# Performance work log

Measured on AMD Instinct MI355X. Metric: run time of the kernel, lower is better.

The kernel has to match this reference:

```python
import jax, jax.numpy as jnp
import numpy as np

B, C, H, W = 256, 1024, 7, 7
D_HID, N_CLS = 768, 5

def setup_inputs() -> dict:
    key = jax.random.key(0)
    k1, k2, k3, k4, k5 = jax.random.split(key, 5)
    flat = C * H * W  # 50176
    return {
        "features": jax.random.normal(k1, (B, C, H, W), dtype=jnp.float32),
        "W1": jax.random.normal(k2, (D_HID, flat), dtype=jnp.float32) * 0.02,
        "b1": jax.random.normal(k3, (D_HID,), dtype=jnp.float32) * 0.02,
        "W2": jax.random.normal(k4, (N_CLS, D_HID), dtype=jnp.float32) * 0.02,
        "b2": jax.random.normal(k5, (N_CLS,), dtype=jnp.float32) * 0.02,
    }

def reference(features, W1, b1, W2, b2):
    # PCAM: per-(batch, channel) global max over spatial dims, broadcast-multiplied
    # back onto the feature map. Replaces the torch Python double loop with one
    # fused reduce-max + elementwise multiply.
    ch_max = jnp.max(features, axis=(2, 3), keepdims=True)  # [B, C, 1, 1]
    pcams = features * ch_max                               # [B, C, H, W]
    flat = pcams.reshape(pcams.shape[0], -1)                # [B, C*H*W]
    h = jax.nn.relu(flat @ W1.T + b1)                       # [B, 768]
    logits = h @ W2.T + b2                                  # [B, num_classes]
    return (logits, features)
```

## Files before the change

kernel.cpp:

```cpp
#include <hip/hip_runtime.h>
#include <hip/hip_bf16.h>

#define B_SZ   256
#define C_SZ   1024
#define HW     49
#define KDIM   50176
#define DHID   768
#define NCLS   5

typedef __bf16 bf16x8 __attribute__((ext_vector_type(8)));
typedef __bf16 bf16x4 __attribute__((ext_vector_type(4)));
typedef float  f32x4  __attribute__((ext_vector_type(4)));

#define GLOAD_LDS16(gsrc, ldst) \
  __builtin_amdgcn_global_load_lds((__attribute__((address_space(1))) void*)(gsrc), \
                                   (__attribute__((address_space(3))) void*)(ldst), 16, 0, 0)

__global__ __launch_bounds__(256) void pcam_kernel(const float* __restrict__ feat,
                                                   float* __restrict__ feat_out,
                                                   __bf16* __restrict__ pcam) {
  __shared__ float sv[1568];
  __shared__ float smax[32];
  const int tid = threadIdx.x;
  const size_t base = (size_t)blockIdx.x * 1568;

  const float4* src4 = (const float4*)(feat + base);
  float4* dst4 = (float4*)(feat_out + base);
  #pragma unroll
  for (int i = 0; i < 2; ++i) {
    int idx = tid + i * 256;
    if (idx < 392) {
      float4 v = src4[idx];
      dst4[idx] = v;
      ((float4*)sv)[idx] = v;
    }
  }
  __syncthreads();

  {
    const int r = tid >> 3, p = tid & 7;
    float mx = -INFINITY;
    for (int i = p; i < HW; i += 8) mx = fmaxf(mx, sv[r * HW + i]);
    #pragma unroll
    for (int off = 1; off < 8; off <<= 1) mx = fmaxf(mx, __shfl_xor(mx, off));
    if (p == 0) smax[r] = mx;
  }
  __syncthreads();

  for (int i = tid; i < 1568; i += 256) {
    int r = (i * 1338) >> 16;
    float v = sv[i] * smax[r];
    pcam[base + i] = (__bf16)v;
  }
}

#define BM 256
#define BN 128
#define BK 64
#define NT 6
#define KSPLIT 42
#define KSTEPS 784

__global__ __launch_bounds__(512, 2) void gemm1_kernel(const __bf16* __restrict__ pcam,
                                                       const float* __restrict__ W1,
                                                       float* __restrict__ h_acc) {
  __shared__ __bf16 Asm[BM * BK];
  __shared__ __bf16 Bsm[BN * BK];

  const int tid  = threadIdx.x;
  const int lane = tid & 63;
  const int w    = tid >> 6;
  const int wm   = w >> 1;
  const int wn   = w & 1;
  const int n0   = blockIdx.x * BN;
  const int ks   = blockIdx.y;
  const int s0   = (ks * KSTEPS) / KSPLIT;
  const int s1   = ((ks + 1) * KSTEPS) / KSPLIT;

  f32x4 acc[4][4];
  #pragma unroll
  for (int i = 0; i < 4; ++i)
    #pragma unroll
    for (int j = 0; j < 4; ++j) acc[i][j] = f32x4{0.f, 0.f, 0.f, 0.f};

  for (int s = s0; s < s1; ++s) {
    const int k0 = s * BK;

    #pragma unroll
    for (int it = 0; it < 4; ++it) {
      const int q   = it * 512 + tid;
      const int m   = q >> 3;
      const int kbp = q & 7;
      const int kbl = kbp ^ (m & 7);
      const __bf16* src = pcam + (size_t)m * KDIM + k0 + kbl * 8;
      __bf16* ldsb = Asm + (size_t)(it * 512 + w * 64) * 8;
      GLOAD_LDS16(src, ldsb);
    }

    #pragma unroll
    for (int it = 0; it < 4; ++it) {
      const int f  = it * 512 + tid;
      const int n  = f >> 4;
      const int kq = f & 15;
      const float4 v = *(const float4*)(W1 + (size_t)(n0 + n) * KDIM + k0 + kq * 4);
      bf16x4 bv;
      bv[0] = (__bf16)v.x; bv[1] = (__bf16)v.y; bv[2] = (__bf16)v.z; bv[3] = (__bf16)v.w;
      const int kb   = kq >> 1;
      const int phys = n * 128 + (((kb ^ (n & 7)) << 4) | ((kq & 1) << 3));
      *(bf16x4*)((char*)Bsm + phys) = bv;
    }
    __syncthreads();

    #pragma unroll
    for (int ksub = 0; ksub < 2; ++ksub) {
      bf16x8 af[4], bfr[4];
      const int kb = ksub * 4 + (lane >> 4);
      #pragma unroll
      for (int i = 0; i < 4; ++i) {
        const int m = wm * 64 + i * 16 + (lane & 15);
        af[i] = *(const bf16x8*)((const char*)Asm + m * 128 + ((kb ^ (m & 7)) << 4));
      }
      #pragma unroll
      for (int j = 0; j < 4; ++j) {
        const int n = wn * 64 + j * 16 + (lane & 15);
        bfr[j] = *(const bf16x8*)((const char*)Bsm + n * 128 + ((kb ^ (n & 7)) << 4));
      }
      #pragma unroll
      for (int i = 0; i < 4; ++i)
        #pragma unroll
        for (int j = 0; j < 4; ++j)
          acc[i][j] = __builtin_amdgcn_mfma_f32_16x16x32_bf16(af[i], bfr[j], acc[i][j], 0, 0, 0);
    }
    __syncthreads();
  }

  #pragma unroll
  for (int i = 0; i < 4; ++i) {
    const int mb = wm * 64 + i * 16 + (lane >> 4) * 4;
    #pragma unroll
    for (int j = 0; j < 4; ++j) {
      const int n = n0 + wn * 64 + j * 16 + (lane & 15);
      #pragma unroll
      for (int r = 0; r < 4; ++r)
        unsafeAtomicAdd(&h_acc[(size_t)(mb + r) * DHID + n], acc[i][j][r]);
    }
  }
}

__global__ __launch_bounds__(64) void head_kernel(const float* __restrict__ h_acc,
                                                  const float* __restrict__ b1,
                                                  const float* __restrict__ W2,
                                                  const float* __restrict__ b2,
                                                  float* __restrict__ logits) {
  const int m = blockIdx.x;
  const int lane = threadIdx.x;
  float hv[12];
  #pragma unroll
  for (int j = 0; j < 12; ++j) {
    float v = h_acc[(size_t)m * DHID + j * 64 + lane] + b1[j * 64 + lane];
    hv[j] = v > 0.f ? v : 0.f;
  }
  #pragma unroll
  for (int c = 0; c < NCLS; ++c) {
    float s = 0.f;
    #pragma unroll
    for (int j = 0; j < 12; ++j) s += hv[j] * W2[c * DHID + j * 64 + lane];
    #pragma unroll
    for (int off = 32; off > 0; off >>= 1) s += __shfl_xor(s, off);
    if (lane == 0) logits[m * NCLS + c] = s + b2[c];
  }
}

extern "C" void kernel_launch(void* const* d_in, const int* in_sizes, int n_in,
                              void* d_out, int out_size, void* d_ws, size_t ws_size,
                              hipStream_t stream) {
  const float* feat = (const float*)d_in[0];
  const float* W1   = (const float*)d_in[1];
  const float* b1   = (const float*)d_in[2];
  const float* W2   = (const float*)d_in[3];
  const float* b2   = (const float*)d_in[4];

  float* logits   = (float*)d_out;
  float* feat_out = (float*)d_out + (size_t)B_SZ * NCLS;

  __bf16* pcam  = (__bf16*)d_ws;
  float*  h_acc = (float*)((char*)d_ws + (size_t)B_SZ * KDIM * 2);

  hipMemsetAsync(h_acc, 0, (size_t)B_SZ * DHID * sizeof(float), stream);
  pcam_kernel<<<(B_SZ * C_SZ) / 32, 256, 0, stream>>>(feat, feat_out, pcam);
  gemm1_kernel<<<dim3(NT, KSPLIT), 512, 0, stream>>>(pcam, W1, h_acc);
  head_kernel<<<B_SZ, 64, 0, stream>>>(h_acc, b1, W2, b2, logits);
}
```

Baseline: 109.3 us.

## Double-buffer GEMM LDS stages and split M into two tiles

The GEMM now uses a 128x128 block tile instead of 256x128, which doubles the grid to 12x42 blocks. It also double-buffers A and B in LDS, prefetching the next k-step (an async global->LDS load for A, a register load for W1) while the current step computes. The goal is to hide global-memory latency and raise occupancy (launch bounds 512,4) for this memory-bound fp32-W1 stream. The cost is that each W1 tile is now read by two blocks, and the extra blocks issue more atomic adds.

Result: slower. 112.4 us (+2.8%).

```diff
diff --git a/kernel.cpp b/kernel.cpp
--- a/kernel.cpp
+++ b/kernel.cpp
@@ -54,97 +54,133 @@
   }
 }
 
-#define BM 256
+#define BM 128
 #define BN 128
 #define BK 64
+#define MT 2
 #define NT 6
 #define KSPLIT 42
 #define KSTEPS 784
 
-__global__ __launch_bounds__(512, 2) void gemm1_kernel(const __bf16* __restrict__ pcam,
+__global__ __launch_bounds__(512, 4) void gemm1_kernel(const __bf16* __restrict__ pcam,
                                                        const float* __restrict__ W1,
                                                        float* __restrict__ h_acc) {
-  __shared__ __bf16 Asm[BM * BK];
-  __shared__ __bf16 Bsm[BN * BK];
+  __shared__ __bf16 Asm[2][BM * BK];
+  __shared__ __bf16 Bsm[2][BN * BK];
 
   const int tid  = threadIdx.x;
   const int lane = tid & 63;
   const int w    = tid >> 6;
-  const int wm   = w >> 1;
-  const int wn   = w & 1;
-  const int n0   = blockIdx.x * BN;
+  const int wm   = w >> 2;
+  const int wn   = w & 3;
+  const int bx   = blockIdx.x;
+  const int m0   = (bx & 1) * BM;
+  const int n0   = (bx >> 1) * BN;
   const int ks   = blockIdx.y;
   const int s0   = (ks * KSTEPS) / KSPLIT;
   const int s1   = ((ks + 1) * KSTEPS) / KSPLIT;
 
-  f32x4 acc[4][4];
+  const int nb = tid >> 4;
+  const int kq = tid & 15;
+  const int kb = kq >> 1;
+  const int sub = (kq & 1) << 3;
+
+  f32x4 acc[4][2];
   #pragma unroll
   for (int i = 0; i < 4; ++i)
     #pragma unroll
-    for (int j = 0; j < 4; ++j) acc[i][j] = f32x4{0.f, 0.f, 0.f, 0.f};
-
+    for (int j = 0; j < 2; ++j) acc[i][j] = f32x4{0.f, 0.f, 0.f, 0.f};
+
+  float4 br0, br1, br2, br3;
+
+#define LOAD_B(s) do { \
+    const size_t koff_ = (size_t)(s) * BK + kq * 4; \
+    br0 = *(const float4*)(W1 + (size_t)(n0 + 0  + nb) * KDIM + koff_); \
+    br1 = *(const float4*)(W1 + (size_t)(n0 + 32 + nb) * KDIM + koff_); \
+    br2 = *(const float4*)(W1 + (size_t)(n0 + 64 + nb) * KDIM + koff_); \
+    br3 = *(const float4*)(W1 + (size_t)(n0 + 96 + nb) * KDIM + koff_); \
+  } while (0)
+
+#define STAGE_A(bi, s) do { \
+    const int k0_ = (s) * BK; \
+    _Pragma("unroll") \
+    for (int it = 0; it < 2; ++it) { \
+      const int q   = it * 512 + tid; \
+      const int m   = q >> 3; \
+      const int kbl = (q & 7) ^ (m & 7); \
+      const __bf16* src = pcam + (size_t)(m0 + m) * KDIM + k0_ + kbl * 8; \
+      GLOAD_LDS16(src, &Asm[bi][(size_t)(it * 512 + w * 64) * 8]); \
+    } \
+  } while (0)
+
+#define WRITE_B(bi) do { \
+    _Pragma("unroll") \
+    for (int it = 0; it < 4; ++it) { \
+      const float4 v = (it == 0) ? br0 : (it == 1) ? br1 : (it == 2) ? br2 : br3; \
+      bf16x4 bv; \
+      bv[0] = (__bf16)v.x; bv[1] = (__bf16)v.y; bv[2] = (__bf16)v.z; bv[3] = (__bf16)v.w; \
+      const int n = it * 32 + nb; \
+      const int phys = n * 128 + (((kb ^ (n & 7)) << 4) | sub); \
+      *(bf16x4*)((char*)Bsm[bi] + phys) = bv; \
+    } \
+  } while (0)
+
+#define COMPUTE(bi) do { \
+    _Pragma("unroll") \
+    for (int ksub = 0; ksub < 2; ++ksub) { \
+      bf16x8 af[4], bfr[2]; \
+      const int kb2 = ksub * 4 + (lane >> 4); \
+      _Pragma("unroll") \
+      for (int i = 0; i < 4; ++i) { \
+        const int m = wm * 64 + i * 16 + (lane & 15); \
+        af[i] = *(const bf16x8*)((const char*)Asm[bi] + m * 128 + ((kb2 ^ (m & 7)) << 4)); \
+      } \
+      _Pragma("unroll") \
+      for (int j = 0; j < 2; ++j) { \
+        const int n = wn * 32 + j * 16 + (lane & 15); \
+        bfr[j] = *(const bf16x8*)((const char*)Bsm[bi] + n * 128 + ((kb2 ^ (n & 7)) << 4)); \
+      } \
+      _Pragma("unroll") \
+      for (int i = 0; i < 4; ++i) \
+        _Pragma("unroll") \
+        for (int j = 0; j < 2; ++j) \
+          acc[i][j] = __builtin_amdgcn_mfma_f32_16x16x32_bf16(af[i], bfr[j], acc[i][j], 0, 0, 0); \
+    } \
+  } while (0)
+
+  LOAD_B(s0);
+  STAGE_A(0, s0);
+  WRITE_B(0);
+  __syncthreads();
+
+  int buf = 0;
   for (int s = s0; s < s1; ++s) {
-    const int k0 = s * BK;
-
-    #pragma unroll
-    for (int it = 0; it < 4; ++it) {
-      const int q   = it * 512 + tid;
-      const int m   = q >> 3;
-      const int kbp = q & 7;
-      const int kbl = kbp ^ (m & 7);
-      const __bf16* src = pcam + (size_t)m * KDIM + k0 + kbl * 8;
-      __bf16* ldsb = Asm + (size_t)(it * 512 + w * 64) * 8;
-      GLOAD_LDS16(src, ldsb);
+    const int nxt = s + 1;
+    if (nxt < s1) {
+      LOAD_B(nxt);
+      STAGE_A(buf ^ 1, nxt);
     }
-
-    #pragma unroll
-    for (int it = 0; it < 4; ++it) {
-      const int f  = it * 512 + tid;
-      const int n  = f >> 4;
-      const int kq = f & 15;
-      const float4 v = *(const float4*)(W1 + (size_t)(n0 + n) * KDIM + k0 + kq * 4);
-      bf16x4 bv;
-      bv[0] = (__bf16)v.x; bv[1] = (__bf16)v.y; bv[2] = (__bf16)v.z; bv[3] = (__bf16)v.w;
-      const int kb   = kq >> 1;
-      const int phys = n * 128 + (((kb ^ (n & 7)) << 4) | ((kq & 1) << 3));
-      *(bf16x4*)((char*)Bsm + phys) = bv;
-    }
+    COMPUTE(buf);
+    if (nxt < s1) WRITE_B(buf ^ 1);
     __syncthreads();
-
-    #pragma unroll
-    for (int ksub = 0; ksub < 2; ++ksub) {
-      bf16x8 af[4], bfr[4];
-      const int kb = ksub * 4 + (lane >> 4);
-      #pragma unroll
-      for (int i = 0; i < 4; ++i) {
-        const int m = wm * 64 + i * 16 + (lane & 15);
-        af[i] = *(const bf16x8*)((const char*)Asm + m * 128 + ((kb ^ (m & 7)) << 4));
-      }
-      #pragma unroll
-      for (int j = 0; j < 4; ++j) {
-        const int n = wn * 64 + j * 16 + (lane & 15);
-        bfr[j] = *(const bf16x8*)((const char*)Bsm + n * 128 + ((kb ^ (n & 7)) << 4));
-      }
-      #pragma unroll
-      for (int i = 0; i < 4; ++i)
-        #pragma unroll
-        for (int j = 0; j < 4; ++j)
-          acc[i][j] = __builtin_amdgcn_mfma_f32_16x16x32_bf16(af[i], bfr[j], acc[i][j], 0, 0, 0);
-    }
-    __syncthreads();
+    buf ^= 1;
   }
 
   #pragma unroll
   for (int i = 0; i < 4; ++i) {
-    const int mb = wm * 64 + i * 16 + (lane >> 4) * 4;
-    #pragma unroll
-    for (int j = 0; j < 4; ++j) {
-      const int n = n0 + wn * 64 + j * 16 + (lane & 15);
+    const int mb = m0 + wm * 64 + i * 16 + (lane >> 4) * 4;
+    #pragma unroll
+    for (int j = 0; j < 2; ++j) {
+      const int n = n0 + wn * 32 + j * 16 + (lane & 15);
       #pragma unroll
       for (int r = 0; r < 4; ++r)
         unsafeAtomicAdd(&h_acc[(size_t)(mb + r) * DHID + n], acc[i][j][r]);
     }
   }
+#undef LOAD_B
+#undef STAGE_A
+#undef WRITE_B
+#undef COMPUTE
 }
 
 __global__ __launch_bounds__(64) void head_kernel(const float* __restrict__ h_acc,
@@ -188,6 +224,6 @@
 
   hipMemsetAsync(h_acc, 0, (size_t)B_SZ * DHID * sizeof(float), stream);
   pcam_kernel<<<(B_SZ * C_SZ) / 32, 256, 0, stream>>>(feat, feat_out, pcam);
-  gemm1_kernel<<<dim3(NT, KSPLIT), 512, 0, stream>>>(pcam, W1, h_acc);
+  gemm1_kernel<<<dim3(MT * NT, KSPLIT), 512, 0, stream>>>(pcam, W1, h_acc);
   head_kernel<<<B_SZ, 64, 0, stream>>>(h_acc, b1, W2, b2, logits);
 }
```

## Retile GEMM1, load fp32 W1 directly into LDS, replace atomics with split-K reduce

Applied to the files above, without the earlier changes.

The GEMM tile shrinks to 128x128 with 256 threads and the grid grows to 12x64 blocks. W1 now goes into LDS through async global_load_lds as fp32 and is converted to bf16 when fragments are read, instead of a register round-trip. Split-K partials are written to a workspace buffer and summed by a new reduce kernel that also applies bias and ReLU, which replaces the atomics and the memset. In exchange, W1 is now read twice (once per M-tile), LDS traffic and the conversion work grow, and there is an extra kernel launch plus 50MB of partial-sum traffic.

Result: slower. 115.5 us (+5.7%).

```diff
diff --git a/kernel.cpp b/kernel.cpp
--- a/kernel.cpp
+++ b/kernel.cpp
@@ -9,7 +9,6 @@
 #define NCLS   5
 
 typedef __bf16 bf16x8 __attribute__((ext_vector_type(8)));
-typedef __bf16 bf16x4 __attribute__((ext_vector_type(4)));
 typedef float  f32x4  __attribute__((ext_vector_type(4)));
 
 #define GLOAD_LDS16(gsrc, ldst) \
@@ -54,101 +53,123 @@
   }
 }
 
-#define BM 256
+#define BM 128
 #define BN 128
 #define BK 64
+#define MT 2
 #define NT 6
-#define KSPLIT 42
+#define KSPLIT 64
 #define KSTEPS 784
 
-__global__ __launch_bounds__(512, 2) void gemm1_kernel(const __bf16* __restrict__ pcam,
+__global__ __launch_bounds__(256, 3) void gemm1_kernel(const __bf16* __restrict__ pcam,
                                                        const float* __restrict__ W1,
-                                                       float* __restrict__ h_acc) {
+                                                       float* __restrict__ h_part) {
   __shared__ __bf16 Asm[BM * BK];
-  __shared__ __bf16 Bsm[BN * BK];
+  __shared__ float  Bsm[BN * BK];
 
   const int tid  = threadIdx.x;
   const int lane = tid & 63;
   const int w    = tid >> 6;
   const int wm   = w >> 1;
   const int wn   = w & 1;
-  const int n0   = blockIdx.x * BN;
+  const int bx   = blockIdx.x;
+  const int m0   = (bx & 1) * BM;
+  const int n0   = (bx >> 1) * BN;
   const int ks   = blockIdx.y;
   const int s0   = (ks * KSTEPS) / KSPLIT;
   const int s1   = ((ks + 1) * KSTEPS) / KSPLIT;
 
+  unsigned a_off[4];
+  #pragma unroll
+  for (int it = 0; it < 4; ++it) {
+    const unsigned ug = it * 256 + tid;
+    const unsigned m  = ug >> 3;
+    a_off[it] = (unsigned)(m0 + m) * KDIM + (((ug & 7) ^ (m & 7)) * 8u);
+  }
+  unsigned b_off[8];
+  #pragma unroll
+  for (int it = 0; it < 8; ++it) {
+    const unsigned ug = it * 256 + tid;
+    const unsigned r  = ug >> 4;
+    const unsigned up = ug & 15;
+    b_off[it] = (unsigned)(n0 + r) * KDIM + (((up >> 1) ^ (r & 7)) * 8u) + ((up & 1) * 4u);
+  }
+
   f32x4 acc[4][4];
   #pragma unroll
   for (int i = 0; i < 4; ++i)
     #pragma unroll
     for (int j = 0; j < 4; ++j) acc[i][j] = f32x4{0.f, 0.f, 0.f, 0.f};
 
+  const int j_ = lane >> 4;
+  const int c_ = lane & 15;
+
   for (int s = s0; s < s1; ++s) {
-    const int k0 = s * BK;
-
-    #pragma unroll
-    for (int it = 0; it < 4; ++it) {
-      const int q   = it * 512 + tid;
-      const int m   = q >> 3;
-      const int kbp = q & 7;
-      const int kbl = kbp ^ (m & 7);
-      const __bf16* src = pcam + (size_t)m * KDIM + k0 + kbl * 8;
-      __bf16* ldsb = Asm + (size_t)(it * 512 + w * 64) * 8;
-      GLOAD_LDS16(src, ldsb);
-    }
-
-    #pragma unroll
-    for (int it = 0; it < 4; ++it) {
-      const int f  = it * 512 + tid;
-      const int n  = f >> 4;
-      const int kq = f & 15;
-      const float4 v = *(const float4*)(W1 + (size_t)(n0 + n) * KDIM + k0 + kq * 4);
-      bf16x4 bv;
-      bv[0] = (__bf16)v.x; bv[1] = (__bf16)v.y; bv[2] = (__bf16)v.z; bv[3] = (__bf16)v.w;
-      const int kb   = kq >> 1;
-      const int phys = n * 128 + (((kb ^ (n & 7)) << 4) | ((kq & 1) << 3));
-      *(bf16x4*)((char*)Bsm + phys) = bv;
-    }
+    const unsigned ka = (unsigned)s * BK;
+    #pragma unroll
+    for (int it = 0; it < 4; ++it)
+      GLOAD_LDS16(pcam + a_off[it] + ka, (char*)Asm + it * 4096 + w * 1024);
+    #pragma unroll
+    for (int it = 0; it < 8; ++it)
+      GLOAD_LDS16(W1 + b_off[it] + ka, (char*)Bsm + it * 4096 + w * 1024);
     __syncthreads();
 
     #pragma unroll
     for (int ksub = 0; ksub < 2; ++ksub) {
-      bf16x8 af[4], bfr[4];
-      const int kb = ksub * 4 + (lane >> 4);
+      const int u = ksub * 4 + j_;
+      bf16x8 af[4];
       #pragma unroll
       for (int i = 0; i < 4; ++i) {
-        const int m = wm * 64 + i * 16 + (lane & 15);
-        af[i] = *(const bf16x8*)((const char*)Asm + m * 128 + ((kb ^ (m & 7)) << 4));
+        const int m = wm * 64 + i * 16 + c_;
+        af[i] = *(const bf16x8*)((const char*)Asm + m * 128 + ((u ^ (m & 7)) << 4));
       }
+      bf16x8 bfr[4];
       #pragma unroll
-      for (int j = 0; j < 4; ++j) {
-        const int n = wn * 64 + j * 16 + (lane & 15);
-        bfr[j] = *(const bf16x8*)((const char*)Bsm + n * 128 + ((kb ^ (n & 7)) << 4));
+      for (int jf = 0; jf < 4; ++jf) {
+        const int r  = wn * 64 + jf * 16 + c_;
+        const int gp = u ^ (r & 7);
+        const f32x4 v0 = *(const f32x4*)((const char*)Bsm + r * 256 + gp * 32);
+        const f32x4 v1 = *(const f32x4*)((const char*)Bsm + r * 256 + gp * 32 + 16);
+        bfr[jf][0] = (__bf16)v0[0]; bfr[jf][1] = (__bf16)v0[1];
+        bfr[jf][2] = (__bf16)v0[2]; bfr[jf][3] = (__bf16)v0[3];
+        bfr[jf][4] = (__bf16)v1[0]; bfr[jf][5] = (__bf16)v1[1];
+        bfr[jf][6] = (__bf16)v1[2]; bfr[jf][7] = (__bf16)v1[3];
       }
       #pragma unroll
       for (int i = 0; i < 4; ++i)
         #pragma unroll
-        for (int j = 0; j < 4; ++j)
-          acc[i][j] = __builtin_amdgcn_mfma_f32_16x16x32_bf16(af[i], bfr[j], acc[i][j], 0, 0, 0);
+        for (int jf = 0; jf < 4; ++jf)
+          acc[i][jf] = __builtin_amdgcn_mfma_f32_16x16x32_bf16(af[i], bfr[jf], acc[i][jf], 0, 0, 0);
     }
     __syncthreads();
   }
 
+  float* out = h_part + (size_t)ks * DHID * B_SZ;
   #pragma unroll
   for (int i = 0; i < 4; ++i) {
-    const int mb = wm * 64 + i * 16 + (lane >> 4) * 4;
-    #pragma unroll
-    for (int j = 0; j < 4; ++j) {
-      const int n = n0 + wn * 64 + j * 16 + (lane & 15);
-      #pragma unroll
-      for (int r = 0; r < 4; ++r)
-        unsafeAtomicAdd(&h_acc[(size_t)(mb + r) * DHID + n], acc[i][j][r]);
+    const int mb = m0 + wm * 64 + i * 16 + j_ * 4;
+    #pragma unroll
+    for (int jf = 0; jf < 4; ++jf) {
+      const int n = n0 + wn * 64 + jf * 16 + c_;
+      *(f32x4*)(out + (size_t)n * B_SZ + mb) = acc[i][jf];
     }
   }
 }
 
-__global__ __launch_bounds__(64) void head_kernel(const float* __restrict__ h_acc,
-                                                  const float* __restrict__ b1,
+__global__ __launch_bounds__(256) void reduce_kernel(const float* __restrict__ h_part,
+                                                     const float* __restrict__ b1,
+                                                     float* __restrict__ h) {
+  const int n = blockIdx.x;
+  const int m = threadIdx.x;
+  float s = 0.f;
+  #pragma unroll 8
+  for (int ks = 0; ks < KSPLIT; ++ks)
+    s += h_part[((size_t)ks * DHID + n) * B_SZ + m];
+  float v = s + b1[n];
+  h[(size_t)m * DHID + n] = v > 0.f ? v : 0.f;
+}
+
+__global__ __launch_bounds__(64) void head_kernel(const float* __restrict__ h,
                                                   const float* __restrict__ W2,
                                                   const float* __restrict__ b2,
                                                   float* __restrict__ logits) {
@@ -156,10 +177,7 @@
   const int lane = threadIdx.x;
   float hv[12];
   #pragma unroll
-  for (int j = 0; j < 12; ++j) {
-    float v = h_acc[(size_t)m * DHID + j * 64 + lane] + b1[j * 64 + lane];
-    hv[j] = v > 0.f ? v : 0.f;
-  }
+  for (int j = 0; j < 12; ++j) hv[j] = h[(size_t)m * DHID + j * 64 + lane];
   #pragma unroll
   for (int c = 0; c < NCLS; ++c) {
     float s = 0.f;
@@ -183,11 +201,14 @@
   float* logits   = (float*)d_out;
   float* feat_out = (float*)d_out + (size_t)B_SZ * NCLS;
 
-  __bf16* pcam  = (__bf16*)d_ws;
-  float*  h_acc = (float*)((char*)d_ws + (size_t)B_SZ * KDIM * 2);
-
-  hipMemsetAsync(h_acc, 0, (size_t)B_SZ * DHID * sizeof(float), stream);
+  char* ws = (char*)d_ws;
+  __bf16* pcam   = (__bf16*)ws;
+  float*  h_part = (float*)(ws + (size_t)B_SZ * KDIM * 2);
+  float*  h      = (float*)(ws + (size_t)B_SZ * KDIM * 2
+                               + (size_t)KSPLIT * DHID * B_SZ * 4);
+
   pcam_kernel<<<(B_SZ * C_SZ) / 32, 256, 0, stream>>>(feat, feat_out, pcam);
-  gemm1_kernel<<<dim3(NT, KSPLIT), 512, 0, stream>>>(pcam, W1, h_acc);
-  head_kernel<<<B_SZ, 64, 0, stream>>>(h_acc, b1, W2, b2, logits);
-}
+  gemm1_kernel<<<dim3(MT * NT, KSPLIT), 256, 0, stream>>>(pcam, W1, h_part);
+  reduce_kernel<<<DHID, 256, 0, stream>>>(h_part, b1, h);
+  head_kernel<<<B_SZ, 64, 0, stream>>>(h, W2, b2, logits);
+}
```
